# Kernel optimization log

Hardware: AMD Instinct MI355X
Metric: run time of the kernel (lower is better)

Reference implementation:

```python
import jax, jax.numpy as jnp
import numpy as np

N_NODES = 100000
N_EDGES = 1600000
HIDDEN = 64
IN_CH = 6  # 3 (direction) + 3 (node feature part)
BN_EPS = 1e-5


def setup_inputs() -> dict:
    key = jax.random.key(0)
    ks = jax.random.split(key, 16)
    inp = {
        "x": jax.random.normal(ks[0], (N_NODES, 3), dtype=jnp.float32),
        "pos": jax.random.normal(ks[1], (N_NODES, 3), dtype=jnp.float32),
        "edge_index": jax.random.randint(ks[2], (2, N_EDGES), 0, N_NODES, dtype=jnp.int64),
    }
    dims = [IN_CH, HIDDEN, HIDDEN, HIDDEN]
    for i in range(3):
        din, dout = dims[i], dims[i + 1]
        inp[f"W{i+1}"] = jax.random.normal(ks[3 + 4 * i], (din, dout), dtype=jnp.float32) * (1.0 / np.sqrt(din))
        inp[f"b{i+1}"] = jnp.zeros((dout,), dtype=jnp.float32)
        inp[f"g{i+1}"] = jnp.ones((dout,), dtype=jnp.float32)   # BN gamma
        inp[f"be{i+1}"] = jnp.zeros((dout,), dtype=jnp.float32)  # BN beta
    return inp


def _mlp_layer(h, W, b, g, be):
    # Linear -> ReLU -> BatchNorm1d (training mode, biased variance like torch)
    h = jax.nn.relu(h @ W + b)
    mu = jnp.mean(h, axis=0)
    var = jnp.mean((h - mu) ** 2, axis=0)
    return g * (h - mu) * jax.lax.rsqrt(var + BN_EPS) + be


def reference(x, pos, edge_index, W1, b1, g1, be1, W2, b2, g2, be2, W3, b3, g3, be3):
    n = x.shape[0]
    xp = jnp.concatenate([pos, x], axis=1)             # [N, 3+F]
    src, dst = edge_index[0], edge_index[1]            # j = src, i = dst (PyG source_to_target)
    x_j = xp[src]                                      # [E, 3+F]
    x_i = xp[dst]
    direction = x_j[:, :3] - x_i[:, :3]                # [E, 3]
    # NOTE: source uses torch.norm with no dim => single global scalar norm
    direction = direction / jnp.linalg.norm(direction)
    h = jnp.concatenate([direction, x_i[:, 3:]], axis=-1)  # [E, IN_CH]
    h = _mlp_layer(h, W1, b1, g1, be1)
    h = _mlp_layer(h, W2, b2, g2, be2)
    h = _mlp_layer(h, W3, b3, g3, be3)                 # [E, HIDDEN]
    out = jax.ops.segment_max(h, dst, num_segments=n)  # scatter-max aggregation
    out = jnp.where(jnp.isfinite(out), out, 0.0)       # PyG fills empty segments with 0
    return out
```

## Files before the change

kernel.cpp:

```cpp
#include <hip/hip_runtime.h>
#include <stdint.h>

typedef unsigned short u16;
typedef unsigned int u32;
typedef __attribute__((ext_vector_type(8))) short short8;
typedef __attribute__((ext_vector_type(4))) float floatx4;

#define BN_EPS 1e-5f
#define NPB 256
#define NBMAX 512

__device__ __forceinline__ float bf2f(u16 u) { return __uint_as_float(((unsigned)u) << 16); }
__device__ __forceinline__ u16 f2bf(float f) {
  unsigned u = __float_as_uint(f);
  u += 0x7FFFu + ((u >> 16) & 1u);
  return (u16)(u >> 16);
}
__device__ __forceinline__ u32 fkey(float f) {
  unsigned u = __float_as_uint(f);
  return (u >> 31) ? ~u : (u | 0x80000000u);
}
__device__ __forceinline__ float funkey(u32 k) {
  return (k & 0x80000000u) ? __uint_as_float(k ^ 0x80000000u) : __uint_as_float(~k);
}

__global__ void k_init(float* __restrict__ stats, u32* __restrict__ bucketTotal) {
  for (int i = threadIdx.x; i < 1024; i += blockDim.x) stats[i] = 0.f;
  for (int i = threadIdx.x; i < NBMAX + 1; i += blockDim.x) bucketTotal[i] = 0u;
}

__global__ void k_norm_hist(const int* __restrict__ ei, const float* __restrict__ pos,
                            int E, int NB, float* __restrict__ stats,
                            u32* __restrict__ bucketTotal) {
  __shared__ u32 lh[NBMAX];
  __shared__ float red[16];
  for (int i = threadIdx.x; i < NB; i += blockDim.x) lh[i] = 0u;
  __syncthreads();
  int tid = blockIdx.x * blockDim.x + threadIdx.x;
  int stride = gridDim.x * blockDim.x;
  float acc = 0.f;
  for (int e = tid; e < E; e += stride) {
    int s = ei[e], d = ei[E + e];
    float d0 = pos[3 * s + 0] - pos[3 * d + 0];
    float d1 = pos[3 * s + 1] - pos[3 * d + 1];
    float d2 = pos[3 * s + 2] - pos[3 * d + 2];
    acc = fmaf(d0, d0, acc);
    acc = fmaf(d1, d1, acc);
    acc = fmaf(d2, d2, acc);
    atomicAdd(&lh[d >> 8], 1u);
  }
#pragma unroll
  for (int off = 32; off > 0; off >>= 1) acc += __shfl_down(acc, off, 64);
  if ((threadIdx.x & 63) == 0) red[threadIdx.x >> 6] = acc;
  __syncthreads();
  if (threadIdx.x == 0) {
    float s = 0.f;
    for (int w = 0; w < (int)(blockDim.x >> 6); w++) s += red[w];
    atomicAdd(&stats[0], s);
  }
  for (int i = threadIdx.x; i < NB; i += blockDim.x)
    if (lh[i]) atomicAdd(&bucketTotal[i], lh[i]);
}

__global__ void k_scan(const u32* __restrict__ bucketTotal, u32* __restrict__ base,
                       u32* __restrict__ cursor, int NB) {
  if (threadIdx.x == 0 && blockIdx.x == 0) {
    u32 run = 0;
    for (int b = 0; b < NB; b++) {
      base[b] = run;
      cursor[b] = run;
      run += bucketTotal[b];
    }
    base[NB] = run;
  }
}

__global__ void k_place(const int* __restrict__ ei, int E, int NB,
                        u32* __restrict__ cursor, u32* __restrict__ sorted) {
  __shared__ u32 lh[NBMAX];
  __shared__ u32 lbase[NBMAX];
  for (int i = threadIdx.x; i < NB; i += blockDim.x) lh[i] = 0u;
  __syncthreads();
  int tid = blockIdx.x * blockDim.x + threadIdx.x;
  int stride = gridDim.x * blockDim.x;
  for (int e = tid; e < E; e += stride) atomicAdd(&lh[ei[E + e] >> 8], 1u);
  __syncthreads();
  for (int i = threadIdx.x; i < NB; i += blockDim.x) {
    u32 c = lh[i];
    lbase[i] = c ? atomicAdd(&cursor[i], c) : 0u;
    lh[i] = 0u;
  }
  __syncthreads();
  for (int e = tid; e < E; e += stride) {
    int d = ei[E + e];
    int b = d >> 8;
    u32 slot = lbase[b] + atomicAdd(&lh[b], 1u);
    sorted[slot] = ((u32)e << 8) | (u32)(d & 255);
  }
}

__global__ __launch_bounds__(512) void k_bucket_max(
    const u32* __restrict__ sorted, const u32* __restrict__ base,
    const u16* __restrict__ h, const float* __restrict__ sc3,
    const float* __restrict__ sh3, float* __restrict__ outf, int N) {
  __shared__ u32 tile[NPB * 64];
  for (int i = threadIdx.x; i < NPB * 64; i += blockDim.x) tile[i] = 0u;
  int b = blockIdx.x;
  u32 start = base[b];
  int cnt = (int)(base[b + 1] - start);
  int t = threadIdx.x;
  int es = t >> 3;
  int c0 = (t & 7) * 8;
  float sc[8], sh[8];
#pragma unroll
  for (int j = 0; j < 8; j++) { sc[j] = sc3[c0 + j]; sh[j] = sh3[c0 + j]; }
  __syncthreads();

  for (int i0 = 0; i0 < cnt; i0 += 256) {
    u32 pk[4];
    uint4 raw[4];
    int ok[4];
#pragma unroll
    for (int u_ = 0; u_ < 4; u_++) {
      int sl = i0 + u_ * 64 + es;
      ok[u_] = sl < cnt;
      pk[u_] = ok[u_] ? sorted[start + sl] : 0u;
    }
#pragma unroll
    for (int u_ = 0; u_ < 4; u_++)
      if (ok[u_]) raw[u_] = *(const uint4*)(h + (long)(pk[u_] >> 8) * 64 + c0);
#pragma unroll
    for (int u_ = 0; u_ < 4; u_++) {
      if (!ok[u_]) continue;
      int ln = (int)(pk[u_] & 255u);
      unsigned w[4] = {raw[u_].x, raw[u_].y, raw[u_].z, raw[u_].w};
      u32 key[8];
#pragma unroll
      for (int p = 0; p < 4; p++) {
        float v0 = bf2f((u16)(w[p] & 0xFFFFu));
        float v1 = bf2f((u16)(w[p] >> 16));
        key[2 * p] = fkey(fmaf(v0, sc[2 * p], sh[2 * p]));
        key[2 * p + 1] = fkey(fmaf(v1, sc[2 * p + 1], sh[2 * p + 1]));
      }
#pragma unroll
      for (int jj = 0; jj < 8; jj++) {
        int j = (jj + es) & 7;
        atomicMax(&tile[ln * 64 + c0 + j], key[j]);
      }
    }
  }
  __syncthreads();
  int node0 = b * NPB;
  for (int l = t; l < NPB * 64; l += blockDim.x) {
    int node = node0 + (l >> 6);
    if (node < N) {
      u32 k = tile[l];
      outf[(long)node * 64 + (l & 63)] = (k == 0u) ? 0.f : funkey(k);
    }
  }
}

__global__ __launch_bounds__(256) void k_layer1(
    const int* __restrict__ ei, const float* __restrict__ pos,
    const float* __restrict__ x, const float* __restrict__ W1,
    const float* __restrict__ b1, u16* __restrict__ h,
    const float* __restrict__ stats, float* __restrict__ gsum,
    float* __restrict__ gsq, int E) {
  __shared__ float in6[6][256];
  __shared__ float ssum[64], ssq[64];
  float invn = 1.0f / sqrtf(stats[0]);
  int t = threadIdx.x;
  int lane = t & 63;
  int wv = t >> 6;
  float w[6];
#pragma unroll
  for (int k = 0; k < 6; k++) w[k] = W1[k * 64 + lane];
  float bias = b1[lane];
  float psum = 0.f, psq = 0.f;

  int chunks = (E + 255) >> 8;
  for (int c = blockIdx.x; c < chunks; c += gridDim.x) {
    long e0 = (long)c << 8;
    int e = (int)e0 + t;
    float v[6] = {0.f, 0.f, 0.f, 0.f, 0.f, 0.f};
    if (e < E) {
      int s = ei[e], d = ei[E + e];
      float p0 = pos[3 * s + 0], p1 = pos[3 * s + 1], p2 = pos[3 * s + 2];
      float q0 = pos[3 * d + 0], q1 = pos[3 * d + 1], q2 = pos[3 * d + 2];
      v[0] = (p0 - q0) * invn;
      v[1] = (p1 - q1) * invn;
      v[2] = (p2 - q2) * invn;
      v[3] = x[3 * d + 0];
      v[4] = x[3 * d + 1];
      v[5] = x[3 * d + 2];
    }
    __syncthreads();
#pragma unroll
    for (int k = 0; k < 6; k++) in6[k][t] = v[k];
    __syncthreads();
    int lim = E - (int)e0;
    if (lim > 256) lim = 256;
    int base = wv * 64;
#pragma unroll 4
    for (int i = 0; i < 64; i++) {
      int el = base + i;
      if (el >= lim) break;
      float acc = bias;
#pragma unroll
      for (int k = 0; k < 6; k++) acc = fmaf(in6[k][el], w[k], acc);
      acc = fmaxf(acc, 0.f);
      u16 hb = f2bf(acc);
      h[(e0 + el) * 64 + lane] = hb;
      float hf = bf2f(hb);
      psum += hf;
      psq = fmaf(hf, hf, psq);
    }
  }
  if (t < 64) { ssum[t] = 0.f; ssq[t] = 0.f; }
  __syncthreads();
  atomicAdd(&ssum[lane], psum);
  atomicAdd(&ssq[lane], psq);
  __syncthreads();
  if (t < 64) {
    atomicAdd(&gsum[t], ssum[t]);
    atomicAdd(&gsq[t], ssq[t]);
  }
}

__global__ void k_fin(const float* __restrict__ gsum, const float* __restrict__ gsq,
                      const float* __restrict__ g, const float* __restrict__ be,
                      float* __restrict__ scale, float* __restrict__ shift, float invE) {
  int c = threadIdx.x;
  float mu = gsum[c] * invE;
  float var = gsq[c] * invE - mu * mu;
  float s = g[c] * rsqrtf(var + BN_EPS);
  scale[c] = s;
  shift[c] = be[c] - mu * s;
}

__global__ __launch_bounds__(256) void k_layer_mfma(
    u16* h, const float* __restrict__ W, const float* __restrict__ b,
    const float* __restrict__ scale_in, const float* __restrict__ shift_in,
    float* __restrict__ gsum, float* __restrict__ gsq, int E) {
  int lane = threadIdx.x & 63;
  int m = lane & 15;
  int q = lane >> 4;

  short8 bf[4][2];
  float bias[4];
#pragma unroll
  for (int t = 0; t < 4; t++) {
    int n = t * 16 + m;
    float bb = b[n];
    for (int k = 0; k < 64; k++) bb = fmaf(shift_in[k], W[k * 64 + n], bb);
    bias[t] = bb;
#pragma unroll
    for (int s = 0; s < 2; s++)
#pragma unroll
      for (int j = 0; j < 8; j++) {
        int k = s * 32 + q * 8 + j;
        bf[t][s][j] = (short)f2bf(W[k * 64 + n] * scale_in[k]);
      }
  }

  float psum[4] = {0.f, 0.f, 0.f, 0.f}, psq[4] = {0.f, 0.f, 0.f, 0.f};

  int tiles = E >> 4;
  int gw = ((int)blockIdx.x * (blockDim.x >> 6)) + (threadIdx.x >> 6);
  int nw = (int)gridDim.x * (blockDim.x >> 6);

  for (int tile = gw; tile < tiles; tile += nw) {
    long e0 = (long)tile * 16;
    const u16* rowp = h + (e0 + m) * 64 + q * 8;
    short8 a0 = *(const short8*)(rowp);
    short8 a1 = *(const short8*)(rowp + 32);
    floatx4 acc[4];
#pragma unroll
    for (int t = 0; t < 4; t++) acc[t] = (floatx4){0.f, 0.f, 0.f, 0.f};
#pragma unroll
    for (int t = 0; t < 4; t++)
      acc[t] = __builtin_amdgcn_mfma_f32_16x16x32_bf16(a0, bf[t][0], acc[t], 0, 0, 0);
#pragma unroll
    for (int t = 0; t < 4; t++)
      acc[t] = __builtin_amdgcn_mfma_f32_16x16x32_bf16(a1, bf[t][1], acc[t], 0, 0, 0);

#pragma unroll
    for (int t = 0; t < 4; t++) {
#pragma unroll
      for (int r = 0; r < 4; r++) {
        float v = acc[t][r] + bias[t];
        v = fmaxf(v, 0.f);
        u16 hb = f2bf(v);
        h[(e0 + q * 4 + r) * 64 + t * 16 + m] = hb;
        float hf = bf2f(hb);
        psum[t] += hf;
        psq[t] = fmaf(hf, hf, psq[t]);
      }
    }
  }

#pragma unroll
  for (int t = 0; t < 4; t++) {
    psum[t] += __shfl_xor(psum[t], 16, 64);
    psum[t] += __shfl_xor(psum[t], 32, 64);
    psq[t] += __shfl_xor(psq[t], 16, 64);
    psq[t] += __shfl_xor(psq[t], 32, 64);
  }
  __shared__ float ssum[64], ssq[64];
  if (threadIdx.x < 64) { ssum[threadIdx.x] = 0.f; ssq[threadIdx.x] = 0.f; }
  __syncthreads();
  if (q == 0) {
#pragma unroll
    for (int t = 0; t < 4; t++) {
      atomicAdd(&ssum[t * 16 + m], psum[t]);
      atomicAdd(&ssq[t * 16 + m], psq[t]);
    }
  }
  __syncthreads();
  if (threadIdx.x < 64) {
    atomicAdd(&gsum[threadIdx.x], ssum[threadIdx.x]);
    atomicAdd(&gsq[threadIdx.x], ssq[threadIdx.x]);
  }
}

__global__ void k_initout(float* __restrict__ outf, long n, float* __restrict__ stats,
                          u32* __restrict__ bucketTotal) {
  long i = (long)blockIdx.x * blockDim.x + threadIdx.x;
  long stride = (long)gridDim.x * blockDim.x;
  for (long j = i; j < n; j += stride) outf[j] = __uint_as_float(0xFF800000u);
  if (i < 1024) stats[i] = 0.f;
  if (i < NBMAX + 1) bucketTotal[i] = 0u;
}
__global__ void k_scatter(const int* __restrict__ ei, const u16* __restrict__ h,
                          const float* __restrict__ scale, const float* __restrict__ shift,
                          float* outf, int E) {
  int lane = threadIdx.x & 63;
  int gw = ((int)blockIdx.x * (blockDim.x >> 6)) + (threadIdx.x >> 6);
  int nw = (int)gridDim.x * (blockDim.x >> 6);
  float sc = scale[lane], sh = shift[lane];
  for (int e = gw; e < E; e += nw) {
    int d = ei[E + e];
    float v = fmaf(bf2f(h[(long)e * 64 + lane]), sc, sh);
    float* addr = outf + (long)d * 64 + lane;
    if (v >= 0.f)
      atomicMax((int*)addr, __float_as_int(v));
    else
      atomicMin((unsigned int*)addr, __float_as_uint(v));
  }
}
__global__ void k_out(float* __restrict__ outf, long n) {
  long i = (long)blockIdx.x * blockDim.x + threadIdx.x;
  long stride = (long)gridDim.x * blockDim.x;
  for (long j = i; j < n; j += stride) {
    float v = outf[j];
    unsigned u = __float_as_uint(v);
    if ((u & 0x7F800000u) == 0x7F800000u) v = 0.f;
    outf[j] = v;
  }
}

extern "C" void kernel_launch(void* const* d_in, const int* in_sizes, int n_in,
                              void* d_out, int out_size, void* d_ws, size_t ws_size,
                              hipStream_t stream) {
  const float* x = (const float*)d_in[0];
  const float* pos = (const float*)d_in[1];
  const int* ei = (const int*)d_in[2];
  const float* W1 = (const float*)d_in[3];
  const float* b1 = (const float*)d_in[4];
  const float* g1 = (const float*)d_in[5];
  const float* be1 = (const float*)d_in[6];
  const float* W2 = (const float*)d_in[7];
  const float* b2 = (const float*)d_in[8];
  const float* g2 = (const float*)d_in[9];
  const float* be2 = (const float*)d_in[10];
  const float* W3 = (const float*)d_in[11];
  const float* b3 = (const float*)d_in[12];
  const float* g3 = (const float*)d_in[13];
  const float* be3 = (const float*)d_in[14];

  int N = in_sizes[0] / 3;
  int E = in_sizes[2] / 2;
  int NB = (N + NPB - 1) / NPB;
  long n_out = (long)N * 64;

  char* wsb = (char*)d_ws;
  u16* h = (u16*)wsb;
  size_t off = (size_t)E * 64 * 2;
  float* stats = (float*)(wsb + off);
  off += 1024 * 4;
  u32* bucketTotal = (u32*)(wsb + off);
  off += (NBMAX + 1) * 4;
  u32* baseArr = (u32*)(wsb + off);
  off += (NBMAX + 1) * 4;
  u32* cursor = (u32*)(wsb + off);
  off += NBMAX * 4;
  u32* sorted = (u32*)(wsb + off);
  off += (size_t)E * 4;
  size_t need = off;

  float* gsum1 = stats + 64, * gsq1 = stats + 128;
  float* gsum2 = stats + 192, * gsq2 = stats + 256;
  float* gsum3 = stats + 320, * gsq3 = stats + 384;
  float* sc1 = stats + 512, * sh1 = stats + 576;
  float* sc2 = stats + 640, * sh2 = stats + 704;
  float* sc3 = stats + 768, * sh3 = stats + 832;

  float* outf = (float*)d_out;
  float invE = 1.0f / (float)E;
  bool binned = (ws_size >= need) && (NB <= NBMAX);

  if (binned) {
    k_init<<<1, 1024, 0, stream>>>(stats, bucketTotal);
    k_norm_hist<<<256, 256, 0, stream>>>(ei, pos, E, NB, stats, bucketTotal);
    k_scan<<<1, 64, 0, stream>>>(bucketTotal, baseArr, cursor, NB);
    k_place<<<256, 256, 0, stream>>>(ei, E, NB, cursor, sorted);
    k_layer1<<<1024, 256, 0, stream>>>(ei, pos, x, W1, b1, h, stats, gsum1, gsq1, E);
    k_fin<<<1, 64, 0, stream>>>(gsum1, gsq1, g1, be1, sc1, sh1, invE);
    k_layer_mfma<<<1024, 256, 0, stream>>>(h, W2, b2, sc1, sh1, gsum2, gsq2, E);
    k_fin<<<1, 64, 0, stream>>>(gsum2, gsq2, g2, be2, sc2, sh2, invE);
    k_layer_mfma<<<1024, 256, 0, stream>>>(h, W3, b3, sc2, sh2, gsum3, gsq3, E);
    k_fin<<<1, 64, 0, stream>>>(gsum3, gsq3, g3, be3, sc3, sh3, invE);
    k_bucket_max<<<NB, 512, 0, stream>>>(sorted, baseArr, h, sc3, sh3, outf, N);
  } else {
    k_initout<<<4096, 256, 0, stream>>>(outf, n_out, stats, bucketTotal);
    k_norm_hist<<<256, 256, 0, stream>>>(ei, pos, E, NB <= NBMAX ? NB : 1, stats, bucketTotal);
    k_layer1<<<1024, 256, 0, stream>>>(ei, pos, x, W1, b1, h, stats, gsum1, gsq1, E);
    k_fin<<<1, 64, 0, stream>>>(gsum1, gsq1, g1, be1, sc1, sh1, invE);
    k_layer_mfma<<<1024, 256, 0, stream>>>(h, W2, b2, sc1, sh1, gsum2, gsq2, E);
    k_fin<<<1, 64, 0, stream>>>(gsum2, gsq2, g2, be2, sc2, sh2, invE);
    k_layer_mfma<<<1024, 256, 0, stream>>>(h, W3, b3, sc2, sh2, gsum3, gsq3, E);
    k_fin<<<1, 64, 0, stream>>>(gsum3, gsq3, g3, be3, sc3, sh3, invE);
    k_scatter<<<2048, 256, 0, stream>>>(ei, h, sc3, sh3, outf, E);
    k_out<<<2048, 256, 0, stream>>>(outf, n_out);
  }
}
```

Baseline: 517.2 us.

## Fuse BN finalize into consumers, shrink scatter-max buckets, parallelize bucket scan

Removes the three single-block k_fin launches by recomputing BatchNorm scale and shift inside each consuming kernel (the MFMA layers, the bucket max and the scatter). Buckets shrink from 256 to 64 nodes, which gives about 4x more blocks with a 16KB LDS tile and 256 threads for the bucket-max stage. The serial one-thread prefix scan becomes a wave-wide shuffle scan. The costs are redundant per-block stats math and more buckets in the histogram and place kernels, whose shared-memory arrays grow to 2048 entries.

```diff
diff --git a/kernel.cpp b/kernel.cpp
--- a/kernel.cpp
+++ b/kernel.cpp
@@ -7,8 +7,9 @@
 typedef __attribute__((ext_vector_type(4))) float floatx4;
 
 #define BN_EPS 1e-5f
-#define NPB 256
-#define NBMAX 512
+#define NPB 64
+#define NPB_SHIFT 6
+#define NBMAX 2048
 
 __device__ __forceinline__ float bf2f(u16 u) { return __uint_as_float(((unsigned)u) << 16); }
 __device__ __forceinline__ u16 f2bf(float f) {
@@ -47,7 +48,7 @@
     acc = fmaf(d0, d0, acc);
     acc = fmaf(d1, d1, acc);
     acc = fmaf(d2, d2, acc);
-    atomicAdd(&lh[d >> 8], 1u);
+    atomicAdd(&lh[d >> NPB_SHIFT], 1u);
   }
 #pragma unroll
   for (int off = 32; off > 0; off >>= 1) acc += __shfl_down(acc, off, 64);
@@ -64,15 +65,22 @@
 
 __global__ void k_scan(const u32* __restrict__ bucketTotal, u32* __restrict__ base,
                        u32* __restrict__ cursor, int NB) {
-  if (threadIdx.x == 0 && blockIdx.x == 0) {
-    u32 run = 0;
-    for (int b = 0; b < NB; b++) {
-      base[b] = run;
-      cursor[b] = run;
-      run += bucketTotal[b];
-    }
-    base[NB] = run;
-  }
+  int lane = threadIdx.x;
+  u32 run = 0;
+  for (int b0 = 0; b0 < NB; b0 += 64) {
+    int b = b0 + lane;
+    u32 v = (b < NB) ? bucketTotal[b] : 0u;
+    u32 s = v;
+#pragma unroll
+    for (int off = 1; off < 64; off <<= 1) {
+      u32 t = __shfl_up(s, off, 64);
+      if (lane >= off) s += t;
+    }
+    u32 excl = run + s - v;
+    if (b < NB) { base[b] = excl; cursor[b] = excl; }
+    run += __shfl(s, 63, 64);
+  }
+  if (lane == 0) base[NB] = run;
 }
 
 __global__ void k_place(const int* __restrict__ ei, int E, int NB,
@@ -83,7 +91,7 @@
   __syncthreads();
   int tid = blockIdx.x * blockDim.x + threadIdx.x;
   int stride = gridDim.x * blockDim.x;
-  for (int e = tid; e < E; e += stride) atomicAdd(&lh[ei[E + e] >> 8], 1u);
+  for (int e = tid; e < E; e += stride) atomicAdd(&lh[ei[E + e] >> NPB_SHIFT], 1u);
   __syncthreads();
   for (int i = threadIdx.x; i < NB; i += blockDim.x) {
     u32 c = lh[i];
@@ -93,16 +101,17 @@
   __syncthreads();
   for (int e = tid; e < E; e += stride) {
     int d = ei[E + e];
-    int b = d >> 8;
+    int b = d >> NPB_SHIFT;
     u32 slot = lbase[b] + atomicAdd(&lh[b], 1u);
-    sorted[slot] = ((u32)e << 8) | (u32)(d & 255);
-  }
-}
-
-__global__ __launch_bounds__(512) void k_bucket_max(
+    sorted[slot] = ((u32)e << 8) | (u32)(d & (NPB - 1));
+  }
+}
+
+__global__ __launch_bounds__(256) void k_bucket_max(
     const u32* __restrict__ sorted, const u32* __restrict__ base,
-    const u16* __restrict__ h, const float* __restrict__ sc3,
-    const float* __restrict__ sh3, float* __restrict__ outf, int N) {
+    const u16* __restrict__ h, const float* __restrict__ gsum3,
+    const float* __restrict__ gsq3, const float* __restrict__ g3,
+    const float* __restrict__ be3, float invE, float* __restrict__ outf, int N) {
   __shared__ u32 tile[NPB * 64];
   for (int i = threadIdx.x; i < NPB * 64; i += blockDim.x) tile[i] = 0u;
   int b = blockIdx.x;
@@ -113,16 +122,24 @@
   int c0 = (t & 7) * 8;
   float sc[8], sh[8];
 #pragma unroll
-  for (int j = 0; j < 8; j++) { sc[j] = sc3[c0 + j]; sh[j] = sh3[c0 + j]; }
-  __syncthreads();
-
-  for (int i0 = 0; i0 < cnt; i0 += 256) {
+  for (int j = 0; j < 8; j++) {
+    int c = c0 + j;
+    float mu = gsum3[c] * invE;
+    float var = gsq3[c] * invE - mu * mu;
+    float s = g3[c] * rsqrtf(var + BN_EPS);
+    sc[j] = s;
+    sh[j] = be3[c] - mu * s;
+  }
+  __syncthreads();
+
+  const int SLOTS = 32;
+  for (int i0 = 0; i0 < cnt; i0 += SLOTS * 4) {
     u32 pk[4];
     uint4 raw[4];
     int ok[4];
 #pragma unroll
     for (int u_ = 0; u_ < 4; u_++) {
-      int sl = i0 + u_ * 64 + es;
+      int sl = i0 + u_ * SLOTS + es;
       ok[u_] = sl < cnt;
       pk[u_] = ok[u_] ? sorted[start + sl] : 0u;
     }
@@ -132,7 +149,7 @@
 #pragma unroll
     for (int u_ = 0; u_ < 4; u_++) {
       if (!ok[u_]) continue;
-      int ln = (int)(pk[u_] & 255u);
+      int ln = (int)(pk[u_] & (u32)(NPB - 1));
       unsigned w[4] = {raw[u_].x, raw[u_].y, raw[u_].z, raw[u_].w};
       u32 key[8];
 #pragma unroll
@@ -227,21 +244,22 @@
   }
 }
 
-__global__ void k_fin(const float* __restrict__ gsum, const float* __restrict__ gsq,
-                      const float* __restrict__ g, const float* __restrict__ be,
-                      float* __restrict__ scale, float* __restrict__ shift, float invE) {
-  int c = threadIdx.x;
-  float mu = gsum[c] * invE;
-  float var = gsq[c] * invE - mu * mu;
-  float s = g[c] * rsqrtf(var + BN_EPS);
-  scale[c] = s;
-  shift[c] = be[c] - mu * s;
-}
-
 __global__ __launch_bounds__(256) void k_layer_mfma(
     u16* h, const float* __restrict__ W, const float* __restrict__ b,
-    const float* __restrict__ scale_in, const float* __restrict__ shift_in,
+    const float* __restrict__ gsum_in, const float* __restrict__ gsq_in,
+    const float* __restrict__ g_in, const float* __restrict__ be_in, float invE,
     float* __restrict__ gsum, float* __restrict__ gsq, int E) {
+  __shared__ float sc_s[64], sh_s[64];
+  if (threadIdx.x < 64) {
+    int c = threadIdx.x;
+    float mu = gsum_in[c] * invE;
+    float var = gsq_in[c] * invE - mu * mu;
+    float s = g_in[c] * rsqrtf(var + BN_EPS);
+    sc_s[c] = s;
+    sh_s[c] = be_in[c] - mu * s;
+  }
+  __syncthreads();
+
   int lane = threadIdx.x & 63;
   int m = lane & 15;
   int q = lane >> 4;
@@ -252,14 +270,14 @@
   for (int t = 0; t < 4; t++) {
     int n = t * 16 + m;
     float bb = b[n];
-    for (int k = 0; k < 64; k++) bb = fmaf(shift_in[k], W[k * 64 + n], bb);
+    for (int k = 0; k < 64; k++) bb = fmaf(sh_s[k], W[k * 64 + n], bb);
     bias[t] = bb;
 #pragma unroll
     for (int s = 0; s < 2; s++)
 #pragma unroll
       for (int j = 0; j < 8; j++) {
         int k = s * 32 + q * 8 + j;
-        bf[t][s][j] = (short)f2bf(W[k * 64 + n] * scale_in[k]);
+        bf[t][s][j] = (short)f2bf(W[k * 64 + n] * sc_s[k]);
       }
   }
 
@@ -332,12 +350,16 @@
   if (i < NBMAX + 1) bucketTotal[i] = 0u;
 }
 __global__ void k_scatter(const int* __restrict__ ei, const u16* __restrict__ h,
-                          const float* __restrict__ scale, const float* __restrict__ shift,
-                          float* outf, int E) {
+                          const float* __restrict__ gsum3, const float* __restrict__ gsq3,
+                          const float* __restrict__ g3, const float* __restrict__ be3,
+                          float invE, float* outf, int E) {
   int lane = threadIdx.x & 63;
   int gw = ((int)blockIdx.x * (blockDim.x >> 6)) + (threadIdx.x >> 6);
   int nw = (int)gridDim.x * (blockDim.x >> 6);
-  float sc = scale[lane], sh = shift[lane];
+  float mu = gsum3[lane] * invE;
+  float var = gsq3[lane] * invE - mu * mu;
+  float sc = g3[lane] * rsqrtf(var + BN_EPS);
+  float sh = be3[lane] - mu * sc;
   for (int e = gw; e < E; e += nw) {
     int d = ei[E + e];
     float v = fmaf(bf2f(h[(long)e * 64 + lane]), sc, sh);
@@ -401,9 +423,6 @@
   float* gsum1 = stats + 64, * gsq1 = stats + 128;
   float* gsum2 = stats + 192, * gsq2 = stats + 256;
   float* gsum3 = stats + 320, * gsq3 = stats + 384;
-  float* sc1 = stats + 512, * sh1 = stats + 576;
-  float* sc2 = stats + 640, * sh2 = stats + 704;
-  float* sc3 = stats + 768, * sh3 = stats + 832;
 
   float* outf = (float*)d_out;
   float invE = 1.0f / (float)E;
@@ -415,22 +434,16 @@
     k_scan<<<1, 64, 0, stream>>>(bucketTotal, baseArr, cursor, NB);
     k_place<<<256, 256, 0, stream>>>(ei, E, NB, cursor, sorted);
     k_layer1<<<1024, 256, 0, stream>>>(ei, pos, x, W1, b1, h, stats, gsum1, gsq1, E);
-    k_fin<<<1, 64, 0, stream>>>(gsum1, gsq1, g1, be1, sc1, sh1, invE);
-    k_layer_mfma<<<1024, 256, 0, stream>>>(h, W2, b2, sc1, sh1, gsum2, gsq2, E);
-    k_fin<<<1, 64, 0, stream>>>(gsum2, gsq2, g2, be2, sc2, sh2, invE);
-    k_layer_mfma<<<1024, 256, 0, stream>>>(h, W3, b3, sc2, sh2, gsum3, gsq3, E);
-    k_fin<<<1, 64, 0, stream>>>(gsum3, gsq3, g3, be3, sc3, sh3, invE);
-    k_bucket_max<<<NB, 512, 0, stream>>>(sorted, baseArr, h, sc3, sh3, outf, N);
+    k_layer_mfma<<<1024, 256, 0, stream>>>(h, W2, b2, gsum1, gsq1, g1, be1, invE, gsum2, gsq2, E);
+    k_layer_mfma<<<1024, 256, 0, stream>>>(h, W3, b3, gsum2, gsq2, g2, be2, invE, gsum3, gsq3, E);
+    k_bucket_max<<<NB, 256, 0, stream>>>(sorted, baseArr, h, gsum3, gsq3, g3, be3, invE, outf, N);
   } else {
     k_initout<<<4096, 256, 0, stream>>>(outf, n_out, stats, bucketTotal);
     k_norm_hist<<<256, 256, 0, stream>>>(ei, pos, E, NB <= NBMAX ? NB : 1, stats, bucketTotal);
     k_layer1<<<1024, 256, 0, stream>>>(ei, pos, x, W1, b1, h, stats, gsum1, gsq1, E);
-    k_fin<<<1, 64, 0, stream>>>(gsum1, gsq1, g1, be1, sc1, sh1, invE);
-    k_layer_mfma<<<1024, 256, 0, stream>>>(h, W2, b2, sc1, sh1, gsum2, gsq2, E);
-    k_fin<<<1, 64, 0, stream>>>(gsum2, gsq2, g2, be2, sc2, sh2, invE);
-    k_layer_mfma<<<1024, 256, 0, stream>>>(h, W3, b3, sc2, sh2, gsum3, gsq3, E);
-    k_fin<<<1, 64, 0, stream>>>(gsum3, gsq3, g3, be3, sc3, sh3, invE);
-    k_scatter<<<2048, 256, 0, stream>>>(ei, h, sc3, sh3, outf, E);
+    k_layer_mfma<<<1024, 256, 0, stream>>>(h, W2, b2, gsum1, gsq1, g1, be1, invE, gsum2, gsq2, E);
+    k_layer_mfma<<<1024, 256, 0, stream>>>(h, W3, b3, gsum2, gsq2, g2, be2, invE, gsum3, gsq3, E);
+    k_scatter<<<2048, 256, 0, stream>>>(ei, h, gsum3, gsq3, g3, be3, invE, outf, E);
     k_out<<<2048, 256, 0, stream>>>(outf, n_out);
   }
 }
```

After: 485.4 us. -6.2%, faster.
